# Performance work log

Hardware: AMD Instinct MI355X
Metric: run time of the kernel (lower is better)

Reference implementation:

```python
import jax, jax.numpy as jnp
import numpy as np

SIG = 512                                   # sigSize
NA = 45                                     # numAngles
SQRT2 = float(np.sqrt(2.0))
DIAG = int(np.ceil(SQRT2 * SIG))            # 725, padded (circle=False) size
PAD = int(np.ceil(SQRT2 * SIG - SIG))       # 213
PAD_BEFORE = (SIG + PAD) // 2 - SIG // 2    # 106
THETA = jnp.asarray(np.deg2rad(np.linspace(0.0, 180.0, NA, endpoint=False)), dtype=jnp.float32)


def _rotate_all(img):
    """Bilinear grid_sample rotation (align_corners=True, zero padding) for all angles.
    img: (B, D, D) -> (B, A, D, D)."""
    D = img.shape[-1]
    c = jnp.linspace(-1.0, 1.0, D, dtype=img.dtype)
    xg = c[None, None, :]                    # column coord j
    yg = c[None, :, None]                    # row coord i
    ct = jnp.cos(THETA)[:, None, None]
    st = jnp.sin(THETA)[:, None, None]
    # affine_grid with R = [[c, s, 0], [-s, c, 0]]
    xs = ct * xg + st * yg                   # (A, D, D)
    ys = -st * xg + ct * yg
    px = (xs + 1.0) * 0.5 * (D - 1)
    py = (ys + 1.0) * 0.5 * (D - 1)
    x0 = jnp.floor(px)
    y0 = jnp.floor(py)
    wx = px - x0
    wy = py - y0
    x0i = x0.astype(jnp.int32)
    y0i = y0.astype(jnp.int32)

    def tap(xi, yi, w):
        valid = (xi >= 0) & (xi < D) & (yi >= 0) & (yi < D)
        xi = jnp.clip(xi, 0, D - 1)
        yi = jnp.clip(yi, 0, D - 1)
        return img[:, yi, xi] * (w * valid)[None]

    return (tap(x0i, y0i, (1 - wx) * (1 - wy)) + tap(x0i + 1, y0i, wx * (1 - wy))
            + tap(x0i, y0i + 1, (1 - wx) * wy) + tap(x0i + 1, y0i + 1, wx * wy))


def radon(x):
    """fmult: x (B,1,S,S) -> sinogram (B,1,D,A), circle=False."""
    xp = jnp.pad(x[:, 0], ((0, 0), (PAD_BEFORE, PAD - PAD_BEFORE), (PAD_BEFORE, PAD - PAD_BEFORE)))
    rot = _rotate_all(xp)                    # (B, A, D, D)
    sino = rot.sum(axis=2)                   # ray-sum over rows -> (B, A, D)
    return jnp.transpose(sino, (0, 2, 1))[:, None]   # (B, 1, D, A)


def iradon(sino):
    """ftran: unfiltered backprojection. sino (B,1,D,A) -> (B,1,S,S)."""
    B, _, D, A = sino.shape
    c = jnp.linspace(-1.0, 1.0, D, dtype=sino.dtype)
    ct = jnp.cos(THETA)[:, None, None]
    st = jnp.sin(THETA)[:, None, None]
    t = ct * c[None, None, :] - st * c[None, :, None]     # (A, D, D) detector coord
    pt = (t + 1.0) * 0.5 * (D - 1)
    t0 = jnp.floor(pt)
    wt = pt - t0
    t0i = t0.astype(jnp.int32)
    s = jnp.transpose(sino[:, 0], (0, 2, 1))               # (B, A, D)

    def tap(ti, w):
        valid = (ti >= 0) & (ti < D)
        tic = jnp.clip(ti, 0, D - 1)
        v = jnp.take_along_axis(s, tic.reshape(1, A, D * D), axis=2).reshape(B, A, D, D)
        return v * (w * valid)[None]

    acc = tap(t0i, 1.0 - wt) + tap(t0i + 1, wt)
    reco = acc.sum(axis=1)                                 # sum over angles
    reco = reco[:, PAD_BEFORE:PAD_BEFORE + SIG, PAD_BEFORE:PAD_BEFORE + SIG]
    return (reco * (jnp.pi / (2.0 * A)))[:, None]


def setup_inputs() -> dict:
    key = jax.random.key(0)
    k1, k2 = jax.random.split(key)
    x = jax.random.normal(k1, (2, 1, SIG, SIG), dtype=jnp.float32)
    y = jax.random.normal(k2, (2, 1, DIAG, NA), dtype=jnp.float32)
    return {"x": x, "y": y}


def reference(x, y):
    # CTClass.grad: per-sample ftran(fmult(x_i) - y_i), vectorized over batch
    return iradon(radon(x) - y)
```

## Files before the change

### kernel.cpp

```cpp
#include <hip/hip_runtime.h>
#include <math.h>

#define SIG 512
#define NA 45
#define DD 725
#define PB 106
#define HALFF 362.0f
#define PI_D 3.14159265358979323846

#define TD2 32
#define TY2 32
#define NT2 23
#define NC42 13
#define RW2 52
#define RH2 47
#define NREG2 640
#define NTILES2 (2 * NA * NT2 * NT2)
#define TGRP (NT2 * NT2)

#define ZSTR 728
#define ZELEMS (2 * NA * ZSTR)
#define TBLOFF ZELEMS
#define DESCOFF 65616
#define DESCI 12
#define BMOFF (DESCOFF + NTILES2 * DESCI)
#define BMWORDS 1492
#define WS_NEED ((BMOFF + BMWORDS) * 4)
#define WS_TBL ((TBLOFF + 2 * NA) * 4)

#define NZB 256
#define NSB 186

#define SEGW 52

__device__ __forceinline__ float cidx(int i) {
    return -1.0f + (float)i * (2.0f / 724.0f);
}

__device__ __forceinline__ void ref_trig(int a, float& ct, float& st) {
    float thf = (float)((double)(4 * a) * PI_D / 180.0);
    ct = (float)cos((double)thf);
    st = (float)sin((double)thf);
}

__device__ __forceinline__ bool tile_geom(
    int a, int b, int td, int ty, float ct, float st,
    int& dlohi, int& gcb, int& grb, int& nrows, int& kske, int& y0i,
    int& zbase, int& boff, float& pxbase, float& pybase) {
    float X0 = HALFF * (1.0f - ct - st);
    float Y0 = HALFF * (1.0f + st - ct);
    int d0 = td * TD2, dmax = min(d0 + TD2 - 1, DD - 1);
    int y0 = ty * TY2, ymax = min(y0 + TY2 - 1, DD - 1);
    const float lo = (float)(PB - 1), hi = (float)(PB + SIG);

    float Ax0 = fmaf(ct, (float)d0, X0), Ax1 = fmaf(ct, (float)dmax, X0);
    float Axlo = fminf(Ax0, Ax1), Axhi = fmaxf(Ax0, Ax1);
    float Ay0 = fmaf(-st, (float)d0, Y0), Ay1 = fmaf(-st, (float)dmax, Y0);
    float Aylo = fminf(Ay0, Ay1), Ayhi = fmaxf(Ay0, Ay1);
    float ylo = (float)y0, yhi = (float)ymax;
    if (st > 1e-6f) {
        ylo = fmaxf(ylo, (lo - Axhi) / st - 1.0f);
        yhi = fminf(yhi, (hi - Axlo) / st + 1.0f);
    } else if (Axhi <= lo || Axlo >= hi) { return false; }
    if (ct > 1e-6f) {
        ylo = fmaxf(ylo, (lo - Ayhi) / ct - 1.0f);
        yhi = fminf(yhi, (hi - Aylo) / ct + 1.0f);
    } else if (ct < -1e-6f) {
        ylo = fmaxf(ylo, (hi - Aylo) / ct - 1.0f);
        yhi = fminf(yhi, (lo - Ayhi) / ct + 1.0f);
    } else if (Ayhi <= lo || Aylo >= hi) { return false; }
    int yclo = max(y0, (int)ceilf(ylo));
    int ychi = min(ymax, (int)floorf(yhi));
    if (ychi < yclo) return false;
    float yclof = (float)yclo, ychif = (float)ychi;

    float dloF = (float)d0, dhiF = (float)dmax;
    if (ct > 1e-6f) {
        dloF = fmaxf(dloF, (lo - st * ychif - X0) / ct - 1.0f);
        dhiF = fminf(dhiF, (hi - st * yclof - X0) / ct + 1.0f);
    } else if (ct < -1e-6f) {
        dloF = fmaxf(dloF, (hi - st * yclof - X0) / ct - 1.0f);
        dhiF = fminf(dhiF, (lo - st * ychif - X0) / ct + 1.0f);
    }
    if (st > 1e-6f) {
        float yl2 = (ct >= 0.0f) ? yclof : ychif;
        float yh2 = (ct >= 0.0f) ? ychif : yclof;
        dloF = fmaxf(dloF, (Y0 + ct * yl2 - hi) / st - 1.0f);
        dhiF = fminf(dhiF, (Y0 + ct * yh2 - lo) / st + 1.0f);
    }
    int dclo = max(d0, (int)ceilf(dloF));
    int dchi = min(dmax, (int)floorf(dhiF));
    if (dchi < dclo) return false;

    float pxmin = 1e30f, pxmax = -1e30f, pymin = 1e30f, pymax = -1e30f;
    for (int ci = 0; ci < 4; ++ci) {
        float df = (float)((ci & 1) ? dchi : dclo);
        float yf = (float)((ci & 2) ? ychi : yclo);
        float px = fmaf(st, yf, fmaf(ct, df, X0));
        float py = fmaf(ct, yf, fmaf(-st, df, Y0));
        pxmin = fminf(pxmin, px); pxmax = fmaxf(pxmax, px);
        pymin = fminf(pymin, py); pymax = fmaxf(pymax, py);
    }
    int cx0 = (int)floorf(pxmin) - 1;
    int cx1 = (int)floorf(pxmax) + 2;
    int ry0 = (int)floorf(pymin) - 1;
    int ry1 = (int)floorf(pymax) + 2;
    if (cx1 < PB || cx0 >= PB + SIG || ry1 < PB || ry0 >= PB + SIG) return false;

    int cx0a = PB + (((cx0 - PB) >> 2) << 2);
    nrows = min(ry1 - ry0 + 1, RH2);
    gcb = cx0a - PB;
    grb = ry0 - PB;
    dlohi = (dclo - d0) | ((dchi - d0) << 8);
    kske = (yclo - y0) | ((ychi - y0) << 8);
    y0i = y0;
    zbase = (b * NA + a) * ZSTR + 1 + d0;
    boff = b * SIG * SIG;
    pxbase = fmaf(ct, (float)d0, X0) - (float)cx0a;
    pybase = fmaf(-st, (float)d0, Y0) - (float)ry0;
    return true;
}

template <int MODE>
__global__ void prep(const float* __restrict__ yin, float* __restrict__ z,
                     float* __restrict__ tbl, float* __restrict__ zpage,
                     int* __restrict__ desc, unsigned* __restrict__ bmap) {
    __shared__ float s_trig[4];
    __shared__ int s_ag[2];
    if (blockIdx.x < NZB) {
        int i = blockIdx.x * blockDim.x + threadIdx.x;
        if (i < 256) zpage[i] = 0.0f;
        if (MODE >= 1 && blockIdx.x == 0 && threadIdx.x < NA) {
            float ct, st;
            ref_trig(threadIdx.x, ct, st);
            tbl[2 * threadIdx.x] = ct;
            tbl[2 * threadIdx.x + 1] = st;
        }
        if (i >= ZELEMS) return;
        int r = i / ZSTR;
        int c = i - r * ZSTR;
        float v = 0.0f;
        if (c >= 1 && c <= DD) {
            int d = c - 1;
            int a = r % NA;
            int b = r / NA;
            v = -yin[(b * DD + d) * NA + a];
        }
        z[i] = v;
        return;
    }
    if (MODE < 2) return;
    int base = (blockIdx.x - NZB) * blockDim.x;
    if (threadIdx.x < 2) {
        int tl = min(base + (int)threadIdx.x * 255, NTILES2 - 1);
        int ag = tl / TGRP;
        s_ag[threadIdx.x] = ag;
        float ct, st;
        ref_trig(ag % NA, ct, st);
        s_trig[2 * threadIdx.x] = ct;
        s_trig[2 * threadIdx.x + 1] = st;
    }
    __syncthreads();
    int tile = base + threadIdx.x;
    bool live = false;
    int dlohi, gcb, grb, nrows, kske, y0i, zbase, boff;
    float pxbase, pybase;
    float ct = 0.0f, st = 0.0f;
    if (tile < NTILES2) {
        int td = tile % NT2; int rest = tile / NT2;
        int ty = rest % NT2;
        int ag = rest / NT2;
        int a = ag % NA;
        int b = ag / NA;
        int sel = (ag == s_ag[0]) ? 0 : 2;
        ct = s_trig[sel]; st = s_trig[sel + 1];
        live = tile_geom(a, b, td, ty, ct, st, dlohi, gcb, grb, nrows, kske,
                         y0i, zbase, boff, pxbase, pybase);
    }
    unsigned long long m = __ballot(live);
    if ((threadIdx.x & 63) == 0) {
        int w = tile >> 5;
        bmap[w] = (unsigned)m;
        bmap[w + 1] = (unsigned)(m >> 32);
    }
    if (!live) return;
    int* dp = desc + tile * DESCI;
    float* fp = (float*)dp;
    dp[0] = dlohi; dp[1] = gcb; dp[2] = grb; dp[3] = nrows;
    dp[4] = kske; fp[5] = pxbase; fp[6] = pybase;
    dp[7] = y0i; dp[8] = zbase; dp[9] = boff;
    fp[10] = ct; fp[11] = st;
}

__device__ __forceinline__ void process_tile32(
    const float* __restrict__ img, const float* __restrict__ zpage,
    float ct, float st,
    int dlohi, int gcb, int grb, int nrows, int kske, int y0i, int zbase,
    float pxbase, float pybase,
    float4* reg4, float* __restrict__ z) {
    float* reg = (float*)reg4;
    int lane = threadIdx.x;

    int nch = (nrows * NC42 + 63) >> 6;
    for (int ch = 0; ch < nch; ++ch) {
        int vi = (ch << 6) + lane;
        int r = vi / NC42;
        int c = vi - r * NC42;
        int gr = grb + r;
        int gc = gcb + (c << 2);
        bool valid = ((unsigned)gr < SIG) & ((unsigned)gc < SIG);
        const float* src = valid ? (img + (gr << 9) + gc) : zpage;
        __builtin_amdgcn_global_load_lds(
            (const __attribute__((address_space(1))) void*)src,
            (__attribute__((address_space(3))) void*)(reg4 + (ch << 6)),
            16, 0, 0);
    }
    __syncthreads();

    int half = lane >> 5;
    int dl = lane & 31;
    int ksb = kske & 255, keb = kske >> 8;
    int dlo = dlohi & 255, dhi = dlohi >> 8;
    int n = keb - ksb + 1;
    int sq = ksb + ((n * half) >> 1);
    int eq = ksb + ((n * (half + 1)) >> 1) - 1;

    float lf = (float)min(max(dl, dlo), dhi);
    float pxd = fmaf(ct, lf, pxbase);
    float pyd = fmaf(-st, lf, pybase);
    float sum = 0.0f;
    float yif = (float)(y0i + sq);
#pragma unroll 4
    for (int k = sq; k <= eq; ++k) {
        float px = fmaf(st, yif, pxd);
        float py = fmaf(ct, yif, pyd);
        float fx = floorf(px), fy = floorf(py);
        float wx = px - fx, wy = py - fy;
        int addr = (int)fmaf(fy, (float)RW2, fx);
        float v00 = reg[addr],       v10 = reg[addr + 1];
        float v01 = reg[addr + RW2], v11 = reg[addr + RW2 + 1];
        float top = fmaf(wx, v10 - v00, v00);
        float bot = fmaf(wx, v11 - v01, v01);
        sum = fmaf(wy, bot - top, sum + top);
        yif += 1.0f;
    }
    sum += __shfl_xor(sum, 32);
    if (half == 0 && dl >= dlo && dl <= dhi) {
        atomicAdd(&z[zbase + dl], sum);
    }
}

template <int PRE, int TBL>
__global__ __launch_bounds__(64) void radon32(const float* __restrict__ x,
                                              const float* __restrict__ zpage,
                                              const float* __restrict__ tbl,
                                              const int* __restrict__ desc,
                                              const unsigned* __restrict__ bmap,
                                              float* __restrict__ z) {
    __shared__ float4 reg4[NREG2];

    if (PRE) {
        unsigned w = bmap[blockIdx.x >> 5];
        if (!((w >> (blockIdx.x & 31)) & 1u)) return;
        const int* dp = desc + blockIdx.x * DESCI;
        const float* fp = (const float*)dp;
        process_tile32(x + dp[9], zpage, fp[10], fp[11],
                       dp[0], dp[1], dp[2], dp[3], dp[4], dp[7], dp[8],
                       fp[5], fp[6], reg4, z);
        return;
    }

    int tile = blockIdx.x;
    int td = tile % NT2; int rest = tile / NT2;
    int ty = rest % NT2; rest /= NT2;
    int a = rest % NA;
    int b = rest / NA;
    float ct, st;
    if (TBL) { ct = tbl[2 * a]; st = tbl[2 * a + 1]; }
    else     { ref_trig(a, ct, st); }
    int dlohi, gcb, grb, nrows, kske, y0i, zbase, boff;
    float pxbase, pybase;
    if (!tile_geom(a, b, td, ty, ct, st, dlohi, gcb, grb, nrows, kske, y0i,
                   zbase, boff, pxbase, pybase)) return;
    process_tile32(x + boff, zpage, ct, st, dlohi, gcb, grb, nrows, kske,
                   y0i, zbase, pxbase, pybase, reg4, z);
}

template <int TBL>
__global__ __launch_bounds__(256) void iradon_t(const float* __restrict__ z,
                                                const float* __restrict__ tbl,
                                                float* __restrict__ out) {
    __shared__ float s_sc[NA], s_st2[NA];
    __shared__ int s_lo[NA];
    __shared__ float s_B[NA * 32];
    __shared__ float s_seg[NA * SEGW];

    int t = threadIdx.x;
    int b = blockIdx.x >> 8;
    int tb = blockIdx.x & 255;
    int i0 = (tb >> 4) << 5;
    int j0 = (tb & 15) << 5;

    if (t < NA) {
        float ct, st;
        if (TBL) { ct = tbl[2 * t]; st = tbl[2 * t + 1]; }
        else     { ref_trig(t, ct, st); }
        float sc = ct * HALFF;
        float st2 = -st * HALFF;
        float cxl = cidx(j0 + PB), cxh = cidx(j0 + 31 + PB);
        float cyl = cidx(i0 + PB), cyh = cidx(i0 + 31 + PB);
        float a00 = fmaf(sc, cxl, fmaf(st2, cyl, 363.0f));
        float a01 = fmaf(sc, cxl, fmaf(st2, cyh, 363.0f));
        float a10 = fmaf(sc, cxh, fmaf(st2, cyl, 363.0f));
        float a11 = fmaf(sc, cxh, fmaf(st2, cyh, 363.0f));
        float mn = fminf(fminf(a00, a01), fminf(a10, a11));
        int lo = (int)floorf(mn) - 1;
        lo = min(max(lo, 0), ZSTR - 1 - SEGW);
        s_sc[t] = sc; s_st2[t] = st2; s_lo[t] = lo;
    }
    __syncthreads();

    for (int s = t; s < NA * 32; s += 256) {
        int a = s >> 5, ii = s & 31;
        s_B[s] = fmaf(s_st2[a], cidx(i0 + ii + PB), 363.0f - (float)s_lo[a]);
    }
    const float* zb = z + b * NA * ZSTR;
    for (int s = t; s < NA * SEGW; s += 256) {
        unsigned a = (unsigned)s / SEGW;
        int idx = s - (int)(a * SEGW);
        s_seg[s] = zb[a * ZSTR + s_lo[a] + idx];
    }
    __syncthreads();

    float cxv = cidx(j0 + (t & 31) + PB);
    int r0 = t >> 5;
    float acc0 = 0.f, acc1 = 0.f, acc2 = 0.f, acc3 = 0.f;
    for (int a = 0; a < NA; ++a) {
        float sc = s_sc[a];
        const float* B = s_B + (a << 5) + r0;
        const float* seg = s_seg + a * SEGW;
#define IR_TAP(ACC, OFF)                                                     \
        {   float af = fmaf(sc, cxv, B[OFF]);                                \
            float fl = floorf(af);                                           \
            float wt = af - fl;                                              \
            int ia = min(max((int)af, 0), SEGW - 2);                         \
            float v0 = seg[ia], v1 = seg[ia + 1];                            \
            ACC = fmaf(wt, v1 - v0, ACC + v0); }
        IR_TAP(acc0, 0)
        IR_TAP(acc1, 8)
        IR_TAP(acc2, 16)
        IR_TAP(acc3, 24)
#undef IR_TAP
    }
    const float sfin = (float)(PI_D / (2.0 * NA));
    int j = j0 + (t & 31);
    int ob = (b << 18) + j;
    out[ob + ((i0 + r0) << 9)]      = acc0 * sfin;
    out[ob + ((i0 + r0 + 8) << 9)]  = acc1 * sfin;
    out[ob + ((i0 + r0 + 16) << 9)] = acc2 * sfin;
    out[ob + ((i0 + r0 + 24) << 9)] = acc3 * sfin;
}

extern "C" void kernel_launch(void* const* d_in, const int* in_sizes, int n_in,
                              void* d_out, int out_size, void* d_ws, size_t ws_size,
                              hipStream_t stream) {
    const float* x = (const float*)d_in[0];
    const float* yin = (const float*)d_in[1];
    float* out = (float*)d_out;
    float* z = (float*)d_ws;
    float* tbl = z + TBLOFF;
    int* desc = (int*)(z + DESCOFF);
    unsigned* bmap = (unsigned*)(z + BMOFF);
    float* zpage = out;

    if (ws_size >= (size_t)WS_NEED) {
        prep<2><<<NZB + NSB, 256, 0, stream>>>(yin, z, tbl, zpage, desc, bmap);
        radon32<1, 1><<<NTILES2, 64, 0, stream>>>(x, zpage, tbl, desc, bmap, z);
        iradon_t<1><<<512, 256, 0, stream>>>(z, tbl, out);
    } else if (ws_size >= (size_t)WS_TBL) {
        prep<1><<<NZB, 256, 0, stream>>>(yin, z, tbl, zpage, nullptr, nullptr);
        radon32<0, 1><<<NTILES2, 64, 0, stream>>>(x, zpage, tbl, nullptr, nullptr, z);
        iradon_t<1><<<512, 256, 0, stream>>>(z, tbl, out);
    } else {
        prep<0><<<NZB, 256, 0, stream>>>(yin, z, nullptr, zpage, nullptr, nullptr);
        radon32<0, 0><<<NTILES2, 64, 0, stream>>>(x, zpage, nullptr, nullptr, nullptr, z);
        iradon_t<0><<<512, 256, 0, stream>>>(z, nullptr, out);
    }
}
```

Measured before the change: 44.07 us.

## Add fast interior-tile load path, incremental ray coords, and 16x16 backprojection tiles

Tiles whose footprint lies entirely inside the image get a precomputed flag bit, which lets them use a bounds-check-free load loop that advances the source pointer incrementally instead of dividing and testing every chunk. The ray-sum loop now steps px/py by adding st/ct rather than recomputing FMAs each iteration. The backprojection kernel is retiled from 32x32 to 16x16 output blocks with one pixel per thread and a narrower 32-wide sinogram segment, which gives four times as many blocks. The costs are more redundant per-block setup and a tighter segment window, and incremental coordinates may drift slightly in float.

```diff
diff --git a/kernel.cpp b/kernel.cpp
--- a/kernel.cpp
+++ b/kernel.cpp
@@ -31,7 +31,7 @@
 #define NZB 256
 #define NSB 186
 
-#define SEGW 52
+#define SEGW2 32
 
 __device__ __forceinline__ float cidx(int i) {
     return -1.0f + (float)i * (2.0f / 724.0f);
@@ -184,6 +184,12 @@
         bmap[w + 1] = (unsigned)(m >> 32);
     }
     if (!live) return;
+    {
+        int nch = (nrows * NC42 + 63) >> 6;
+        int rmax = (nch * 64 - 1) / NC42;
+        if (grb >= 0 && grb + rmax < SIG && gcb >= 0 && gcb + 52 <= SIG)
+            dlohi |= (1 << 16);
+    }
     int* dp = desc + tile * DESCI;
     float* fp = (float*)dp;
     dp[0] = dlohi; dp[1] = gcb; dp[2] = grb; dp[3] = nrows;
@@ -202,25 +208,40 @@
     int lane = threadIdx.x;
 
     int nch = (nrows * NC42 + 63) >> 6;
-    for (int ch = 0; ch < nch; ++ch) {
-        int vi = (ch << 6) + lane;
-        int r = vi / NC42;
-        int c = vi - r * NC42;
-        int gr = grb + r;
-        int gc = gcb + (c << 2);
-        bool valid = ((unsigned)gr < SIG) & ((unsigned)gc < SIG);
-        const float* src = valid ? (img + (gr << 9) + gc) : zpage;
-        __builtin_amdgcn_global_load_lds(
-            (const __attribute__((address_space(1))) void*)src,
-            (__attribute__((address_space(3))) void*)(reg4 + (ch << 6)),
-            16, 0, 0);
+    if (dlohi & (1 << 16)) {
+        int r0 = (lane * 5) >> 6;
+        int c0 = lane - r0 * NC42;
+        const float* src = img + ((grb + r0) << 9) + gcb + (c0 << 2);
+        for (int ch = 0; ch < nch; ++ch) {
+            __builtin_amdgcn_global_load_lds(
+                (const __attribute__((address_space(1))) void*)src,
+                (__attribute__((address_space(3))) void*)(reg4 + (ch << 6)),
+                16, 0, 0);
+            bool cy = (c0 != 0);
+            src += cy ? (5 * SIG - 4) : (4 * SIG + 48);
+            c0 = cy ? (c0 - 1) : (NC42 - 1);
+        }
+    } else {
+        for (int ch = 0; ch < nch; ++ch) {
+            int vi = (ch << 6) + lane;
+            int r = vi / NC42;
+            int c = vi - r * NC42;
+            int gr = grb + r;
+            int gc = gcb + (c << 2);
+            bool valid = ((unsigned)gr < SIG) & ((unsigned)gc < SIG);
+            const float* src = valid ? (img + (gr << 9) + gc) : zpage;
+            __builtin_amdgcn_global_load_lds(
+                (const __attribute__((address_space(1))) void*)src,
+                (__attribute__((address_space(3))) void*)(reg4 + (ch << 6)),
+                16, 0, 0);
+        }
     }
     __syncthreads();
 
     int half = lane >> 5;
     int dl = lane & 31;
     int ksb = kske & 255, keb = kske >> 8;
-    int dlo = dlohi & 255, dhi = dlohi >> 8;
+    int dlo = dlohi & 255, dhi = (dlohi >> 8) & 255;
     int n = keb - ksb + 1;
     int sq = ksb + ((n * half) >> 1);
     int eq = ksb + ((n * (half + 1)) >> 1) - 1;
@@ -228,12 +249,12 @@
     float lf = (float)min(max(dl, dlo), dhi);
     float pxd = fmaf(ct, lf, pxbase);
     float pyd = fmaf(-st, lf, pybase);
+    float yif = (float)(y0i + sq);
+    float px = fmaf(st, yif, pxd);
+    float py = fmaf(ct, yif, pyd);
     float sum = 0.0f;
-    float yif = (float)(y0i + sq);
 #pragma unroll 4
     for (int k = sq; k <= eq; ++k) {
-        float px = fmaf(st, yif, pxd);
-        float py = fmaf(ct, yif, pyd);
         float fx = floorf(px), fy = floorf(py);
         float wx = px - fx, wy = py - fy;
         int addr = (int)fmaf(fy, (float)RW2, fx);
@@ -242,7 +263,7 @@
         float top = fmaf(wx, v10 - v00, v00);
         float bot = fmaf(wx, v11 - v01, v01);
         sum = fmaf(wy, bot - top, sum + top);
-        yif += 1.0f;
+        px += st; py += ct;
     }
     sum += __shfl_xor(sum, 32);
     if (half == 0 && dl >= dlo && dl <= dhi) {
@@ -250,26 +271,27 @@
     }
 }
 
-template <int PRE, int TBL>
+__global__ __launch_bounds__(64) void radon32f(const float* __restrict__ x,
+                                               const float* __restrict__ zpage,
+                                               const int* __restrict__ desc,
+                                               const unsigned* __restrict__ bmap,
+                                               float* __restrict__ z) {
+    __shared__ float4 reg4[NREG2];
+    unsigned w = bmap[blockIdx.x >> 5];
+    if (!((w >> (blockIdx.x & 31)) & 1u)) return;
+    const int* dp = desc + blockIdx.x * DESCI;
+    const float* fp = (const float*)dp;
+    process_tile32(x + dp[9], zpage, fp[10], fp[11],
+                   dp[0], dp[1], dp[2], dp[3], dp[4], dp[7], dp[8],
+                   fp[5], fp[6], reg4, z);
+}
+
+template <int TBL>
 __global__ __launch_bounds__(64) void radon32(const float* __restrict__ x,
                                               const float* __restrict__ zpage,
                                               const float* __restrict__ tbl,
-                                              const int* __restrict__ desc,
-                                              const unsigned* __restrict__ bmap,
                                               float* __restrict__ z) {
     __shared__ float4 reg4[NREG2];
-
-    if (PRE) {
-        unsigned w = bmap[blockIdx.x >> 5];
-        if (!((w >> (blockIdx.x & 31)) & 1u)) return;
-        const int* dp = desc + blockIdx.x * DESCI;
-        const float* fp = (const float*)dp;
-        process_tile32(x + dp[9], zpage, fp[10], fp[11],
-                       dp[0], dp[1], dp[2], dp[3], dp[4], dp[7], dp[8],
-                       fp[5], fp[6], reg4, z);
-        return;
-    }
-
     int tile = blockIdx.x;
     int td = tile % NT2; int rest = tile / NT2;
     int ty = rest % NT2; rest /= NT2;
@@ -287,19 +309,19 @@
 }
 
 template <int TBL>
-__global__ __launch_bounds__(256) void iradon_t(const float* __restrict__ z,
+__global__ __launch_bounds__(256) void iradon16(const float* __restrict__ z,
                                                 const float* __restrict__ tbl,
                                                 float* __restrict__ out) {
     __shared__ float s_sc[NA], s_st2[NA];
     __shared__ int s_lo[NA];
-    __shared__ float s_B[NA * 32];
-    __shared__ float s_seg[NA * SEGW];
+    __shared__ float s_B[NA * 16];
+    __shared__ float s_seg[NA * SEGW2];
 
     int t = threadIdx.x;
-    int b = blockIdx.x >> 8;
-    int tb = blockIdx.x & 255;
-    int i0 = (tb >> 4) << 5;
-    int j0 = (tb & 15) << 5;
+    int b = blockIdx.x >> 10;
+    int tb = blockIdx.x & 1023;
+    int i0 = (tb >> 5) << 4;
+    int j0 = (tb & 31) << 4;
 
     if (t < NA) {
         float ct, st;
@@ -307,58 +329,43 @@
         else     { ref_trig(t, ct, st); }
         float sc = ct * HALFF;
         float st2 = -st * HALFF;
-        float cxl = cidx(j0 + PB), cxh = cidx(j0 + 31 + PB);
-        float cyl = cidx(i0 + PB), cyh = cidx(i0 + 31 + PB);
+        float cxl = cidx(j0 + PB), cxh = cidx(j0 + 15 + PB);
+        float cyl = cidx(i0 + PB), cyh = cidx(i0 + 15 + PB);
         float a00 = fmaf(sc, cxl, fmaf(st2, cyl, 363.0f));
         float a01 = fmaf(sc, cxl, fmaf(st2, cyh, 363.0f));
         float a10 = fmaf(sc, cxh, fmaf(st2, cyl, 363.0f));
         float a11 = fmaf(sc, cxh, fmaf(st2, cyh, 363.0f));
         float mn = fminf(fminf(a00, a01), fminf(a10, a11));
         int lo = (int)floorf(mn) - 1;
-        lo = min(max(lo, 0), ZSTR - 1 - SEGW);
+        lo = min(max(lo, 0), ZSTR - 1 - SEGW2);
         s_sc[t] = sc; s_st2[t] = st2; s_lo[t] = lo;
     }
     __syncthreads();
 
-    for (int s = t; s < NA * 32; s += 256) {
-        int a = s >> 5, ii = s & 31;
+    for (int s = t; s < NA * 16; s += 256) {
+        int a = s >> 4, ii = s & 15;
         s_B[s] = fmaf(s_st2[a], cidx(i0 + ii + PB), 363.0f - (float)s_lo[a]);
     }
     const float* zb = z + b * NA * ZSTR;
-    for (int s = t; s < NA * SEGW; s += 256) {
-        unsigned a = (unsigned)s / SEGW;
-        int idx = s - (int)(a * SEGW);
+    for (int s = t; s < NA * SEGW2; s += 256) {
+        int a = s >> 5, idx = s & 31;
         s_seg[s] = zb[a * ZSTR + s_lo[a] + idx];
     }
     __syncthreads();
 
-    float cxv = cidx(j0 + (t & 31) + PB);
-    int r0 = t >> 5;
-    float acc0 = 0.f, acc1 = 0.f, acc2 = 0.f, acc3 = 0.f;
+    float cxv = cidx(j0 + (t & 15) + PB);
+    int r0 = t >> 4;
+    float acc = 0.f;
     for (int a = 0; a < NA; ++a) {
-        float sc = s_sc[a];
-        const float* B = s_B + (a << 5) + r0;
-        const float* seg = s_seg + a * SEGW;
-#define IR_TAP(ACC, OFF)                                                     \
-        {   float af = fmaf(sc, cxv, B[OFF]);                                \
-            float fl = floorf(af);                                           \
-            float wt = af - fl;                                              \
-            int ia = min(max((int)af, 0), SEGW - 2);                         \
-            float v0 = seg[ia], v1 = seg[ia + 1];                            \
-            ACC = fmaf(wt, v1 - v0, ACC + v0); }
-        IR_TAP(acc0, 0)
-        IR_TAP(acc1, 8)
-        IR_TAP(acc2, 16)
-        IR_TAP(acc3, 24)
-#undef IR_TAP
+        float af = fmaf(s_sc[a], cxv, s_B[(a << 4) + r0]);
+        float fl = floorf(af);
+        float wt = af - fl;
+        int ia = min(max((int)af, 0), SEGW2 - 2);
+        float v0 = s_seg[(a << 5) + ia], v1 = s_seg[(a << 5) + ia + 1];
+        acc = fmaf(wt, v1 - v0, acc + v0);
     }
     const float sfin = (float)(PI_D / (2.0 * NA));
-    int j = j0 + (t & 31);
-    int ob = (b << 18) + j;
-    out[ob + ((i0 + r0) << 9)]      = acc0 * sfin;
-    out[ob + ((i0 + r0 + 8) << 9)]  = acc1 * sfin;
-    out[ob + ((i0 + r0 + 16) << 9)] = acc2 * sfin;
-    out[ob + ((i0 + r0 + 24) << 9)] = acc3 * sfin;
+    out[(b << 18) + ((i0 + r0) << 9) + j0 + (t & 15)] = acc * sfin;
 }
 
 extern "C" void kernel_launch(void* const* d_in, const int* in_sizes, int n_in,
@@ -375,15 +382,15 @@
 
     if (ws_size >= (size_t)WS_NEED) {
         prep<2><<<NZB + NSB, 256, 0, stream>>>(yin, z, tbl, zpage, desc, bmap);
-        radon32<1, 1><<<NTILES2, 64, 0, stream>>>(x, zpage, tbl, desc, bmap, z);
-        iradon_t<1><<<512, 256, 0, stream>>>(z, tbl, out);
+        radon32f<<<NTILES2, 64, 0, stream>>>(x, zpage, desc, bmap, z);
+        iradon16<1><<<2048, 256, 0, stream>>>(z, tbl, out);
     } else if (ws_size >= (size_t)WS_TBL) {
         prep<1><<<NZB, 256, 0, stream>>>(yin, z, tbl, zpage, nullptr, nullptr);
-        radon32<0, 1><<<NTILES2, 64, 0, stream>>>(x, zpage, tbl, nullptr, nullptr, z);
-        iradon_t<1><<<512, 256, 0, stream>>>(z, tbl, out);
+        radon32<1><<<NTILES2, 64, 0, stream>>>(x, zpage, tbl, z);
+        iradon16<1><<<2048, 256, 0, stream>>>(z, tbl, out);
     } else {
         prep<0><<<NZB, 256, 0, stream>>>(yin, z, nullptr, zpage, nullptr, nullptr);
-        radon32<0, 0><<<NTILES2, 64, 0, stream>>>(x, zpage, nullptr, nullptr, nullptr, z);
-        iradon_t<0><<<512, 256, 0, stream>>>(z, nullptr, out);
-    }
-}
+        radon32<0><<<NTILES2, 64, 0, stream>>>(x, zpage, nullptr, z);
+        iradon16<0><<<2048, 256, 0, stream>>>(z, nullptr, out);
+    }
+}
```

Measured after the change: 40.43 us. 8.3% less time.
